# Kernel tuning notes

Hardware: AMD Instinct MI355X
Metric: run time of the kernel (lower is better)

Reference implementation:

```python
import jax, jax.numpy as jnp
import numpy as np
from jax.ops import segment_sum, segment_max

N = 20000      # nodes
DEG = 16       # incoming edges per node
E = N * DEG    # edges
IN = 128       # in_features
BOND = 16      # bond_features_dim
OUT = 128      # output_features
NUM_LAYERS = 3
LEAKY = 0.2
ELU_ALPHA = 1.0


def _lin_params(key, out_f, in_f):
    kw, kb = jax.random.split(key)
    s = 1.0 / np.sqrt(in_f)
    w = jax.random.uniform(kw, (out_f, in_f), jnp.float32, -s, s)
    b = jax.random.uniform(kb, (out_f,), jnp.float32, -s, s)
    return w, b


def setup_inputs() -> dict:
    key = jax.random.key(0)
    ks = jax.random.split(key, 20)
    atom_features = jax.random.normal(ks[0], (N, IN), jnp.float32)
    edge_src = jax.random.randint(ks[1], (E,), 0, N, jnp.int32)
    # every node receives exactly DEG edges (avoids the isolated-node bug path)
    edge_dst = jnp.repeat(jnp.arange(N, dtype=jnp.int32), DEG)
    bond_features = jax.random.normal(ks[2], (E, BOND), jnp.float32)

    v1_fc1_w, v1_fc1_b = _lin_params(ks[3], OUT, IN)
    v1_fc2_w, v1_fc2_b = _lin_params(ks[4], OUT, IN + BOND)
    v1_att_w, v1_att_b = _lin_params(ks[5], 1, 2 * OUT)
    v1_attend_w, v1_attend_b = _lin_params(ks[6], OUT, OUT)
    v1_gru_wih, v1_gru_bih = _lin_params(ks[7], 3 * OUT, OUT)
    v1_gru_whh, v1_gru_bhh = _lin_params(ks[8], 3 * OUT, OUT)

    v2_fc1_w, v2_fc1_b = _lin_params(ks[9], 1, 2 * OUT)
    v2_fc2_w, v2_fc2_b = _lin_params(ks[10], OUT, OUT)
    v2_gru_wih, v2_gru_bih = _lin_params(ks[11], 3 * OUT, OUT)
    v2_gru_whh, v2_gru_bhh = _lin_params(ks[12], 3 * OUT, OUT)

    lin_w, lin_b = _lin_params(ks[13], OUT, OUT)

    return dict(atom_features=atom_features, edge_src=edge_src, edge_dst=edge_dst,
                bond_features=bond_features,
                v1_fc1_w=v1_fc1_w, v1_fc1_b=v1_fc1_b, v1_fc2_w=v1_fc2_w, v1_fc2_b=v1_fc2_b,
                v1_att_w=v1_att_w, v1_att_b=v1_att_b, v1_attend_w=v1_attend_w, v1_attend_b=v1_attend_b,
                v1_gru_wih=v1_gru_wih, v1_gru_whh=v1_gru_whh, v1_gru_bih=v1_gru_bih, v1_gru_bhh=v1_gru_bhh,
                v2_fc1_w=v2_fc1_w, v2_fc1_b=v2_fc1_b, v2_fc2_w=v2_fc2_w, v2_fc2_b=v2_fc2_b,
                v2_gru_wih=v2_gru_wih, v2_gru_whh=v2_gru_whh, v2_gru_bih=v2_gru_bih, v2_gru_bhh=v2_gru_bhh,
                lin_w=lin_w, lin_b=lin_b)


def _linear(x, w, b):
    return x @ w.T + b


def _gru_cell(x, h, wih, whh, bih, bhh):
    gi = x @ wih.T + bih   # [N, 3*OUT]
    gh = h @ whh.T + bhh
    i_r, i_z, i_n = jnp.split(gi, 3, axis=-1)
    h_r, h_z, h_n = jnp.split(gh, 3, axis=-1)
    r = jax.nn.sigmoid(i_r + h_r)
    z = jax.nn.sigmoid(i_z + h_z)
    n = jnp.tanh(i_n + r * h_n)
    return (1.0 - z) * n + z * h


def _segment_softmax(logits, seg, n):
    m = segment_max(logits, seg, num_segments=n)
    ex = jnp.exp(logits - m[seg])
    den = segment_sum(ex, seg, num_segments=n)
    return ex / den[seg]


def reference(atom_features, edge_src, edge_dst, bond_features,
              v1_fc1_w, v1_fc1_b, v1_fc2_w, v1_fc2_b, v1_att_w, v1_att_b,
              v1_attend_w, v1_attend_b, v1_gru_wih, v1_gru_whh, v1_gru_bih, v1_gru_bhh,
              v2_fc1_w, v2_fc1_b, v2_fc2_w, v2_fc2_b,
              v2_gru_wih, v2_gru_whh, v2_gru_bih, v2_gru_bhh,
              lin_w, lin_b):
    n = atom_features.shape[0]
    lrelu = lambda x: jax.nn.leaky_relu(x, negative_slope=LEAKY)

    # ---- GATlayerV1 ----
    new_atom = lrelu(_linear(atom_features, v1_fc1_w, v1_fc1_b))           # [N, OUT]
    nbr_trans = _linear(new_atom, v1_attend_w, v1_attend_b)                # [N, OUT]
    nbr_in = jnp.concatenate([atom_features[edge_src], bond_features], axis=1)  # [E, IN+BOND]
    nbr = lrelu(_linear(nbr_in, v1_fc2_w, v1_fc2_b))                       # [E, OUT]
    pair = jnp.concatenate([new_atom[edge_dst], nbr], axis=1)              # [E, 2*OUT]
    logits = lrelu(_linear(pair, v1_att_w, v1_att_b))[:, 0]                # [E]
    score = _segment_softmax(logits, edge_dst, n)                          # [E]
    transform = segment_sum(score[:, None] * nbr_trans[edge_src], edge_dst, num_segments=n)
    ctx = jax.nn.elu(transform, alpha=ELU_ALPHA)
    h = _gru_cell(ctx, new_atom, v1_gru_wih, v1_gru_whh, v1_gru_bih, v1_gru_bhh)
    G_0 = new_atom

    all_tensors = [h]

    # ---- GATlayerV2 (shared weights across layers 2..NUM_LAYERS) ----
    for _ in range(NUM_LAYERS - 1):
        nt = _linear(h, v2_fc2_w, v2_fc2_b)                                # [N, OUT]
        pair2 = jnp.concatenate([h[edge_dst], h[edge_src]], axis=1)        # [E, 2*OUT]
        lg = lrelu(_linear(pair2, v2_fc1_w, v2_fc1_b))[:, 0]               # [E]
        sc = _segment_softmax(lg, edge_dst, n)
        tr = segment_sum(sc[:, None] * nt[edge_src], edge_dst, num_segments=n)
        ctx2 = jax.nn.elu(tr, alpha=ELU_ALPHA)
        h = _gru_cell(ctx2, h, v2_gru_wih, v2_gru_whh, v2_gru_bih, v2_gru_bhh)
        all_tensors.append(h)

    all_stack = jnp.stack(all_tensors)           # [NUM_LAYERS, N, OUT]
    averaged = all_stack.mean(axis=0)            # [N, OUT]
    output = jax.nn.gelu(_linear(averaged, lin_w, lin_b), approximate=False)
    return (output, all_stack, G_0, averaged)
```

## Files before the change

### kernel.cpp

```cpp
#include <hip/hip_runtime.h>
#include <math.h>

#define NN 20000
#define EE 320000

using short8 = __attribute__((ext_vector_type(8))) short;
using f32x4  = __attribute__((ext_vector_type(4))) float;
using u16x4  = __attribute__((ext_vector_type(4))) unsigned short;

__device__ __forceinline__ unsigned short f2bf(float x) {
    union { float f; unsigned u; } v; v.f = x;
    unsigned r = (v.u + 0x7fffu + ((v.u >> 16) & 1u)) >> 16;
    return (unsigned short)r;
}
__device__ __forceinline__ float bf2f(unsigned short b) {
    union { unsigned u; float f; } v; v.u = ((unsigned)b) << 16;
    return v.f;
}
__device__ __forceinline__ float sigmoidf_(float x) { return 1.f / (1.f + __expf(-x)); }
__device__ __forceinline__ float tanhf_(float x) {
    float e = __expf(-2.f * x);
    return (1.f - e) / (1.f + e);
}
__device__ __forceinline__ float lrelu_(float x) { return x > 0.f ? x : 0.2f * x; }
__device__ __forceinline__ float elu_(float x) { return x > 0.f ? x : __expf(x) - 1.f; }

struct PackDesc { const float* w; unsigned short* out; int O; int ldw; int mode; };
struct PackArgs { PackDesc d[10]; };

__global__ void k_pack(PackArgs args) {
    PackDesc d = args.d[blockIdx.y];
    int idx = blockIdx.x * 256 + threadIdx.x;
    if (d.mode == 1) {
        if (idx >= 512) return;
        int t = idx >> 6, l = idx & 63;
        int lr = l & 15, lg = l >> 4;
        int ch = lr * 8 + t;
        short8 o;
        #pragma unroll
        for (int j = 0; j < 8; j++) {
            int k = lg * 8 + j;
            o[j] = (k < 16) ? (short)f2bf(d.w[(size_t)ch * 144 + 128 + k]) : (short)0;
        }
        *(short8*)(d.out + (size_t)idx * 8) = o;
        return;
    }
    int total = (d.O / 16) * 4 * 64;
    if (idx >= total) return;
    int l = idx & 63, rest = idx >> 6;
    int ko = rest & 3, no = rest >> 2;
    int row = no * 16 + (l & 15);
    int col0 = ko * 32 + ((l >> 4) * 8);
    const float* src = d.w + (size_t)row * d.ldw + col0;
    unsigned short o[8];
    #pragma unroll
    for (int j = 0; j < 8; j++) o[j] = f2bf(src[j]);
    #pragma unroll
    for (int j = 0; j < 8; j++) d.out[(size_t)idx * 8 + j] = o[j];
}

__global__ __launch_bounds__(256) void k_v1_front(
    const float* __restrict__ atom,
    const unsigned short* __restrict__ Bfc1, const unsigned short* __restrict__ BW2a,
    const float* __restrict__ fc1_b, const float* __restrict__ fc2_b,
    const float* __restrict__ attw,
    float* __restrict__ g0, unsigned short* __restrict__ naBf,
    unsigned short* __restrict__ Ubf, float* __restrict__ adst)
{
    __shared__ float Xs[16][132];
    __shared__ unsigned short Ys2[16 * 128];
    const int tid = threadIdx.x, l = tid & 63, w = tid >> 6;
    const int lr = l & 15, lg = l >> 4;
    const int m0 = blockIdx.x * 16;

    f32x4 acc1[2] = {}, accU[2] = {};
    #pragma unroll
    for (int ko = 0; ko < 4; ko++) {
        const f32x4* ap = (const f32x4*)(atom + (size_t)(m0 + lr) * 128 + ko * 32 + lg * 8);
        f32x4 a0 = ap[0], a1 = ap[1];
        short8 af;
        #pragma unroll
        for (int j = 0; j < 4; j++) { af[j] = (short)f2bf(a0[j]); af[4 + j] = (short)f2bf(a1[j]); }
        #pragma unroll
        for (int i = 0; i < 2; i++) {
            int t = w * 2 + i;
            short8 b1 = *(const short8*)(Bfc1 + ((size_t)(t * 4 + ko) * 64 + l) * 8);
            acc1[i] = __builtin_amdgcn_mfma_f32_16x16x32_bf16(af, b1, acc1[i], 0, 0, 0);
            short8 bu = *(const short8*)(BW2a + ((size_t)(t * 4 + ko) * 64 + l) * 8);
            accU[i] = __builtin_amdgcn_mfma_f32_16x16x32_bf16(af, bu, accU[i], 0, 0, 0);
        }
    }
    #pragma unroll
    for (int i = 0; i < 2; i++) {
        int col = (w * 2 + i) * 16 + lr;
        float b1v = fc1_b[col], bUv = fc2_b[col];
        #pragma unroll
        for (int r = 0; r < 4; r++) {
            int row = lg * 4 + r;
            float v = lrelu_(acc1[i][r] + b1v);
            Xs[row][col] = v;
            Ys2[row * 128 + col] = f2bf(accU[i][r] + bUv);
        }
    }
    __syncthreads();
    *(short8*)(Ubf + (size_t)m0 * 128 + tid * 8) = *(const short8*)(Ys2 + tid * 8);
    {
        int row = tid >> 4, q = tid & 15;
        short8 tmp;
        float p = 0.f;
        float vv[8];
        #pragma unroll
        for (int j = 0; j < 8; j++) {
            float x = Xs[row][q * 8 + j];
            vv[j] = x;
            tmp[j] = (short)f2bf(x);
            p = fmaf(x, attw[q * 8 + j], p);
        }
        *(f32x4*)(g0 + (size_t)(m0 + row) * 128 + q * 8) = *(f32x4*)vv;
        *(f32x4*)(g0 + (size_t)(m0 + row) * 128 + q * 8 + 4) = *(f32x4*)(vv + 4);
        *(short8*)(naBf + (size_t)(m0 + row) * 128 + q * 8) = tmp;
        #pragma unroll
        for (int m = 1; m <= 8; m <<= 1) p += __shfl_xor(p, m, 16);
        if (q == 0) adst[m0 + row] = p;
    }
}

template<int AGGMODE, int FRONT, int FINAL>
__global__ __launch_bounds__(512, 4) void k_gru(
    const float* __restrict__ aD, const float* __restrict__ bS, const float* __restrict__ b1,
    const float* __restrict__ bond, const unsigned short* __restrict__ BW2b,
    const float* __restrict__ attw, const float* __restrict__ attb1,
    const float* __restrict__ adst, const unsigned short* __restrict__ U,
    const int* __restrict__ esrc, const unsigned short* __restrict__ V,
    const unsigned short* __restrict__ Bpre, const float* __restrict__ bpre,
    const unsigned short* __restrict__ Bih, const unsigned short* __restrict__ Bhh,
    const float* __restrict__ bih, const float* __restrict__ bhh,
    const unsigned short* __restrict__ hprevBf, float* __restrict__ houtF,
    unsigned short* __restrict__ houtBf,
    const float* __restrict__ w2att, float* __restrict__ aDOut, float* __restrict__ bSOut,
    const float* __restrict__ as0, const float* __restrict__ as1,
    const unsigned short* __restrict__ Blin, const float* __restrict__ linb,
    float* __restrict__ avgOut, float* __restrict__ outF)
{
    __shared__ unsigned short aggS[32][136];
    __shared__ unsigned short ctxS[32][136];
    __shared__ unsigned short hpS[32][136];
    __shared__ float hoS[32][132];
    __shared__ float lgS[32][16];
    const int tid = threadIdx.x, l = tid & 63, w = tid >> 6;
    const int lr = l & 15, lg = l >> 4;
    const int m0 = blockIdx.x * 32;
    const int srow = tid >> 4, sc0 = (tid & 15) * 8;

    *(short8*)&hpS[srow][sc0] = *(const short8*)(hprevBf + (size_t)(m0 + srow) * 128 + sc0);

    if (AGGMODE == 0) {
        float aw[8];
        #pragma unroll
        for (int t = 0; t < 8; t++) aw[t] = attw[128 + lr * 8 + t];
        const float ab = attb1[0];
        #pragma unroll
        for (int nn = 0; nn < 4; nn++) {
            const int n = m0 + w * 4 + nn;
            const int e0 = n * 16;
            short8 af = {};
            if (lg < 2) {
                const f32x4* bp = (const f32x4*)(bond + (size_t)(e0 + lr) * 16 + lg * 8);
                f32x4 b0 = bp[0], b1v = bp[1];
                #pragma unroll
                for (int j = 0; j < 4; j++) {
                    af[j] = (short)f2bf(b0[j]); af[4 + j] = (short)f2bf(b1v[j]);
                }
            }
            f32x4 c[8];
            #pragma unroll
            for (int t = 0; t < 8; t++) {
                short8 bw = *(const short8*)(BW2b + (size_t)(t * 64 + l) * 8);
                f32x4 z = {};
                c[t] = __builtin_amdgcn_mfma_f32_16x16x32_bf16(af, bw, z, 0, 0, 0);
            }
            float s[4];
            #pragma unroll
            for (int r = 0; r < 4; r++) {
                int e = e0 + lg * 4 + r;
                int src = esrc[e];
                short8 u = *(const short8*)(U + (size_t)src * 128 + lr * 8);
                float a0 = 0.f;
                #pragma unroll
                for (int t = 0; t < 8; t++)
                    a0 = fmaf(aw[t], lrelu_(c[t][r] + bf2f((unsigned short)u[t])), a0);
                s[r] = a0;
            }
            #pragma unroll
            for (int mk = 1; mk <= 8; mk <<= 1)
                #pragma unroll
                for (int r = 0; r < 4; r++) s[r] += __shfl_xor(s[r], mk, 16);
            if (lr == 0) {
                float anode = adst[n];
                #pragma unroll
                for (int r = 0; r < 4; r++)
                    lgS[w * 4 + nn][lg * 4 + r] = lrelu_(anode + ab + s[r]);
            }
        }
        __syncthreads();
    }

    {
        const int q = tid & 15;
        const int gnode = m0 + srow;
        const int e = gnode * 16 + q;
        const int src = esrc[e];
        float lgt;
        if (AGGMODE == 0) lgt = lgS[srow][q];
        else              lgt = lrelu_(aD[gnode] + bS[src] + b1[0]);
        float mx = lgt;
        #pragma unroll
        for (int mk = 1; mk <= 8; mk <<= 1) mx = fmaxf(mx, __shfl_xor(mx, mk, 16));
        float ex = __expf(lgt - mx);
        float den = ex;
        #pragma unroll
        for (int mk = 1; mk <= 8; mk <<= 1) den += __shfl_xor(den, mk, 16);
        float wq = ex / den;
        float s[8] = {};
        #pragma unroll
        for (int i = 0; i < 16; i++) {
            float wi = __shfl(wq, i, 16);
            int si = __shfl(src, i, 16);
            const unsigned short* vp = V + (size_t)si * 128 + q * 4;
            u16x4 v0 = *(const u16x4*)vp;
            #pragma unroll
            for (int j = 0; j < 4; j++) s[j] = fmaf(wi, bf2f(v0[j]), s[j]);
            u16x4 v1 = *(const u16x4*)(vp + 64);
            #pragma unroll
            for (int j = 0; j < 4; j++) s[4 + j] = fmaf(wi, bf2f(v1[j]), s[4 + j]);
        }
        u16x4 o0, o1;
        #pragma unroll
        for (int j = 0; j < 4; j++) { o0[j] = f2bf(s[j]); o1[j] = f2bf(s[4 + j]); }
        *(u16x4*)&aggS[srow][q * 4] = o0;
        *(u16x4*)&aggS[srow][64 + q * 4] = o1;
    }
    __syncthreads();

    f32x4 accp[2] = {};
    f32x4 ah[2][3] = {};
    #pragma unroll
    for (int ko = 0; ko < 4; ko++) {
        short8 afA[2], afh[2];
        #pragma unroll
        for (int rt = 0; rt < 2; rt++) {
            afA[rt] = *(const short8*)&aggS[rt * 16 + lr][ko * 32 + lg * 8];
            afh[rt] = *(const short8*)&hpS[rt * 16 + lr][ko * 32 + lg * 8];
        }
        short8 bfp = *(const short8*)(Bpre + ((size_t)(w * 4 + ko) * 64 + l) * 8);
        #pragma unroll
        for (int rt = 0; rt < 2; rt++)
            accp[rt] = __builtin_amdgcn_mfma_f32_16x16x32_bf16(afA[rt], bfp, accp[rt], 0, 0, 0);
        #pragma unroll
        for (int g = 0; g < 3; g++) {
            short8 bh = *(const short8*)(Bhh + ((size_t)((w + 8 * g) * 4 + ko) * 64 + l) * 8);
            #pragma unroll
            for (int rt = 0; rt < 2; rt++)
                ah[rt][g] = __builtin_amdgcn_mfma_f32_16x16x32_bf16(afh[rt], bh, ah[rt][g], 0, 0, 0);
        }
    }
    {
        const int col = w * 16 + lr;
        const float bb = bpre[col];
        #pragma unroll
        for (int rt = 0; rt < 2; rt++)
            #pragma unroll
            for (int r = 0; r < 4; r++)
                ctxS[rt * 16 + lg * 4 + r][col] = f2bf(elu_(accp[rt][r] + bb));
    }
    __syncthreads();

    f32x4 ai[2][3] = {};
    #pragma unroll
    for (int ko = 0; ko < 4; ko++) {
        short8 afc[2];
        #pragma unroll
        for (int rt = 0; rt < 2; rt++)
            afc[rt] = *(const short8*)&ctxS[rt * 16 + lr][ko * 32 + lg * 8];
        #pragma unroll
        for (int g = 0; g < 3; g++) {
            short8 bi = *(const short8*)(Bih + ((size_t)((w + 8 * g) * 4 + ko) * 64 + l) * 8);
            #pragma unroll
            for (int rt = 0; rt < 2; rt++)
                ai[rt][g] = __builtin_amdgcn_mfma_f32_16x16x32_bf16(afc[rt], bi, ai[rt][g], 0, 0, 0);
        }
    }
    {
        const int c = w * 16 + lr;
        const float br = bih[c] + bhh[c];
        const float bz = bih[c + 128] + bhh[c + 128];
        const float bin_ = bih[c + 256];
        const float bhn = bhh[c + 256];
        #pragma unroll
        for (int rt = 0; rt < 2; rt++)
            #pragma unroll
            for (int r = 0; r < 4; r++) {
                const int lrow = rt * 16 + lg * 4 + r;
                float rg = sigmoidf_(ai[rt][0][r] + ah[rt][0][r] + br);
                float zg = sigmoidf_(ai[rt][1][r] + ah[rt][1][r] + bz);
                float ng = tanhf_(ai[rt][2][r] + bin_ + rg * (ah[rt][2][r] + bhn));
                float hp = bf2f(hpS[lrow][c]);
                hoS[lrow][c] = fmaf(zg, hp - ng, ng);
            }
    }
    __syncthreads();

    {
        float v[8];
        #pragma unroll
        for (int k = 0; k < 8; k++) v[k] = hoS[srow][sc0 + k];
        f32x4* dst = (f32x4*)(houtF + (size_t)(m0 + srow) * 128 + sc0);
        dst[0] = *(f32x4*)v;
        dst[1] = *(f32x4*)(v + 4);
        if (FINAL == 0) {
            short8 p;
            #pragma unroll
            for (int k = 0; k < 8; k++) p[k] = (short)f2bf(v[k]);
            *(short8*)(houtBf + (size_t)(m0 + srow) * 128 + sc0) = p;
        }
    }

    if (FRONT) {
        int row = tid >> 4, q = tid & 15;
        float pa = 0.f, pb = 0.f;
        #pragma unroll
        for (int j = 0; j < 8; j++) {
            float x = hoS[row][q * 8 + j];
            pa = fmaf(x, w2att[q * 8 + j], pa);
            pb = fmaf(x, w2att[128 + q * 8 + j], pb);
        }
        #pragma unroll
        for (int m = 1; m <= 8; m <<= 1) {
            pa += __shfl_xor(pa, m, 16);
            pb += __shfl_xor(pb, m, 16);
        }
        if (q == 0) { aDOut[m0 + row] = pa; bSOut[m0 + row] = pb; }
    }

    if (FINAL) {
        {
            const f32x4* p0 = (const f32x4*)(as0 + (size_t)(m0 + srow) * 128 + sc0);
            const f32x4* p1 = (const f32x4*)(as1 + (size_t)(m0 + srow) * 128 + sc0);
            f32x4* pav = (f32x4*)(avgOut + (size_t)(m0 + srow) * 128 + sc0);
            #pragma unroll
            for (int k = 0; k < 2; k++) {
                f32x4 x0 = p0[k], x1 = p1[k];
                f32x4 av;
                #pragma unroll
                for (int j = 0; j < 4; j++)
                    av[j] = (x0[j] + x1[j] + hoS[srow][sc0 + k * 4 + j]) * (1.f / 3.f);
                pav[k] = av;
                #pragma unroll
                for (int j = 0; j < 4; j++) ctxS[srow][sc0 + k * 4 + j] = f2bf(av[j]);
            }
        }
        __syncthreads();
        f32x4 acc2[2] = {};
        #pragma unroll
        for (int ko = 0; ko < 4; ko++) {
            short8 bf = *(const short8*)(Blin + ((size_t)(w * 4 + ko) * 64 + l) * 8);
            #pragma unroll
            for (int rt = 0; rt < 2; rt++) {
                short8 af = *(const short8*)&ctxS[rt * 16 + lr][ko * 32 + lg * 8];
                acc2[rt] = __builtin_amdgcn_mfma_f32_16x16x32_bf16(af, bf, acc2[rt], 0, 0, 0);
            }
        }
        __syncthreads();
        {
            const int col = w * 16 + lr;
            const float bb = linb[col];
            #pragma unroll
            for (int rt = 0; rt < 2; rt++)
                #pragma unroll
                for (int r = 0; r < 4; r++) {
                    float vv = acc2[rt][r] + bb;
                    hoS[rt * 16 + lg * 4 + r][col] =
                        0.5f * vv * (1.f + erff(vv * 0.70710678118654752f));
                }
        }
        __syncthreads();
        {
            float v[8];
            #pragma unroll
            for (int k = 0; k < 8; k++) v[k] = hoS[srow][sc0 + k];
            f32x4* dst = (f32x4*)(outF + (size_t)(m0 + srow) * 128 + sc0);
            dst[0] = *(f32x4*)v;
            dst[1] = *(f32x4*)(v + 4);
        }
    }
}

extern "C" void kernel_launch(void* const* d_in, const int* in_sizes, int n_in,
                              void* d_out, int out_size, void* d_ws, size_t ws_size,
                              hipStream_t stream) {
    const float* atom     = (const float*)d_in[0];
    const int*   esrc     = (const int*)d_in[1];
    const float* bond     = (const float*)d_in[3];
    const float* fc1_w    = (const float*)d_in[4];
    const float* fc1_b    = (const float*)d_in[5];
    const float* fc2_w    = (const float*)d_in[6];
    const float* fc2_b    = (const float*)d_in[7];
    const float* att_w    = (const float*)d_in[8];
    const float* att_b    = (const float*)d_in[9];
    const float* attend_w = (const float*)d_in[10];
    const float* attend_b = (const float*)d_in[11];
    const float* gih1     = (const float*)d_in[12];
    const float* ghh1     = (const float*)d_in[13];
    const float* bih1     = (const float*)d_in[14];
    const float* bhh1     = (const float*)d_in[15];
    const float* fc1v2_w  = (const float*)d_in[16];
    const float* fc1v2_b  = (const float*)d_in[17];
    const float* fc2v2_w  = (const float*)d_in[18];
    const float* fc2v2_b  = (const float*)d_in[19];
    const float* gih2     = (const float*)d_in[20];
    const float* ghh2     = (const float*)d_in[21];
    const float* bih2     = (const float*)d_in[22];
    const float* bhh2     = (const float*)d_in[23];
    const float* lin_w    = (const float*)d_in[24];
    const float* lin_b    = (const float*)d_in[25];

    char* wsb = (char*)d_ws;
    size_t off = 0;
    auto allocB = [&](size_t bytes) {
        size_t o = off; off = (off + bytes + 255) & ~(size_t)255; return o;
    };
    unsigned short* Bfc1   = (unsigned short*)(wsb + allocB(128 * 128 * 2));
    unsigned short* Batt   = (unsigned short*)(wsb + allocB(128 * 128 * 2));
    unsigned short* BW2a   = (unsigned short*)(wsb + allocB(128 * 128 * 2));
    unsigned short* BW2b   = (unsigned short*)(wsb + allocB(512 * 8 * 2));
    unsigned short* Bgih1  = (unsigned short*)(wsb + allocB(384 * 128 * 2));
    unsigned short* Bghh1  = (unsigned short*)(wsb + allocB(384 * 128 * 2));
    unsigned short* Bfc2v2 = (unsigned short*)(wsb + allocB(128 * 128 * 2));
    unsigned short* Bgih2  = (unsigned short*)(wsb + allocB(384 * 128 * 2));
    unsigned short* Bghh2  = (unsigned short*)(wsb + allocB(384 * 128 * 2));
    unsigned short* Blin   = (unsigned short*)(wsb + allocB(128 * 128 * 2));
    unsigned short* naBf   = (unsigned short*)(wsb + allocB((size_t)NN * 128 * 2));
    unsigned short* Ubf    = (unsigned short*)(wsb + allocB((size_t)NN * 128 * 2));
    unsigned short* h1Bf   = (unsigned short*)(wsb + allocB((size_t)NN * 128 * 2));
    unsigned short* h2Bf   = (unsigned short*)(wsb + allocB((size_t)NN * 128 * 2));
    float* adst   = (float*)(wsb + allocB((size_t)NN * 4));
    float* aD     = (float*)(wsb + allocB((size_t)NN * 4));
    float* bS     = (float*)(wsb + allocB((size_t)NN * 4));
    (void)ws_size;

    float* out0 = (float*)d_out;
    float* as0  = out0 + (size_t)NN * 128;
    float* as1  = as0 + (size_t)NN * 128;
    float* as2  = as1 + (size_t)NN * 128;
    float* g0   = out0 + (size_t)4 * NN * 128;
    float* avg  = out0 + (size_t)5 * NN * 128;

    PackArgs pa;
    pa.d[0] = { fc1_w,    Bfc1,   128, 128, 0 };
    pa.d[1] = { attend_w, Batt,   128, 128, 0 };
    pa.d[2] = { fc2_w,    BW2a,   128, 144, 0 };
    pa.d[3] = { gih1,     Bgih1,  384, 128, 0 };
    pa.d[4] = { ghh1,     Bghh1,  384, 128, 0 };
    pa.d[5] = { fc2v2_w,  Bfc2v2, 128, 128, 0 };
    pa.d[6] = { gih2,     Bgih2,  384, 128, 0 };
    pa.d[7] = { ghh2,     Bghh2,  384, 128, 0 };
    pa.d[8] = { lin_w,    Blin,   128, 128, 0 };
    pa.d[9] = { fc2_w,    BW2b,   0,   0,   1 };
    k_pack<<<dim3(24, 10), 256, 0, stream>>>(pa);

    const int GB = NN / 16;
    const int GB32 = NN / 32;

    k_v1_front<<<GB, 256, 0, stream>>>(atom, Bfc1, BW2a, fc1_b, fc2_b, att_w,
                                       g0, naBf, Ubf, adst);
    k_gru<0, 1, 0><<<GB32, 512, 0, stream>>>(
        nullptr, nullptr, nullptr,
        bond, BW2b, att_w, att_b, adst, Ubf,
        esrc, naBf,
        Batt, attend_b,
        Bgih1, Bghh1, bih1, bhh1, naBf, as0, h1Bf,
        fc1v2_w, aD, bS,
        nullptr, nullptr, nullptr, nullptr, nullptr, nullptr);

    k_gru<1, 1, 0><<<GB32, 512, 0, stream>>>(
        aD, bS, fc1v2_b,
        nullptr, nullptr, nullptr, nullptr, nullptr, nullptr,
        esrc, h1Bf,
        Bfc2v2, fc2v2_b,
        Bgih2, Bghh2, bih2, bhh2, h1Bf, as1, h2Bf,
        fc1v2_w, aD, bS,
        nullptr, nullptr, nullptr, nullptr, nullptr, nullptr);

    k_gru<1, 0, 1><<<GB32, 512, 0, stream>>>(
        aD, bS, fc1v2_b,
        nullptr, nullptr, nullptr, nullptr, nullptr, nullptr,
        esrc, h2Bf,
        Bfc2v2, fc2v2_b,
        Bgih2, Bghh2, bih2, bhh2, h2Bf, as2, nullptr,
        nullptr, nullptr, nullptr,
        as0, as1, Blin, lin_b, avg, out0);
}
```

Before: 123.3 us.

## Halve GRU kernel node tile to 16 rows and drop fp32 staging buffer

Each k_gru block now processes 16 nodes instead of 32 with 512 threads, so twice as many blocks launch, registers per thread drop, and launch bounds request 8 blocks per CU. The fp32 hoS shared buffer is removed: the GRU output is written back into hpS as bf16 and reused for outputs, attention projections and the final linear. The aim is higher occupancy and less LDS per block to hide gather latency. The cost is that hidden states and the final output are rounded to bf16 before being written as fp32, which lowers precision, and weight-fragment loads are amortised over fewer rows.

```diff
diff --git a/kernel.cpp b/kernel.cpp
--- a/kernel.cpp
+++ b/kernel.cpp
@@ -126,7 +126,7 @@
 }
 
 template<int AGGMODE, int FRONT, int FINAL>
-__global__ __launch_bounds__(512, 4) void k_gru(
+__global__ __launch_bounds__(512, 8) void k_gru(
     const float* __restrict__ aD, const float* __restrict__ bS, const float* __restrict__ b1,
     const float* __restrict__ bond, const unsigned short* __restrict__ BW2b,
     const float* __restrict__ attw, const float* __restrict__ attb1,
@@ -142,17 +142,16 @@
     const unsigned short* __restrict__ Blin, const float* __restrict__ linb,
     float* __restrict__ avgOut, float* __restrict__ outF)
 {
-    __shared__ unsigned short aggS[32][136];
-    __shared__ unsigned short ctxS[32][136];
-    __shared__ unsigned short hpS[32][136];
-    __shared__ float hoS[32][132];
-    __shared__ float lgS[32][16];
+    __shared__ unsigned short aggS[16][136];
+    __shared__ unsigned short ctxS[16][136];
+    __shared__ unsigned short hpS[16][136];
+    __shared__ float lgS[(AGGMODE == 0) ? 16 : 1][16];
     const int tid = threadIdx.x, l = tid & 63, w = tid >> 6;
     const int lr = l & 15, lg = l >> 4;
-    const int m0 = blockIdx.x * 32;
-    const int srow = tid >> 4, sc0 = (tid & 15) * 8;
-
-    *(short8*)&hpS[srow][sc0] = *(const short8*)(hprevBf + (size_t)(m0 + srow) * 128 + sc0);
+    const int m0 = blockIdx.x * 16;
+    const int r2 = tid >> 5, c4 = (tid & 31) * 4;
+
+    *(u16x4*)&hpS[r2][c4] = *(const u16x4*)(hprevBf + (size_t)(m0 + r2) * 128 + c4);
 
     if (AGGMODE == 0) {
         float aw[8];
@@ -160,8 +159,8 @@
         for (int t = 0; t < 8; t++) aw[t] = attw[128 + lr * 8 + t];
         const float ab = attb1[0];
         #pragma unroll
-        for (int nn = 0; nn < 4; nn++) {
-            const int n = m0 + w * 4 + nn;
+        for (int nn = 0; nn < 2; nn++) {
+            const int n = m0 + w * 2 + nn;
             const int e0 = n * 16;
             short8 af = {};
             if (lg < 2) {
@@ -199,19 +198,22 @@
                 float anode = adst[n];
                 #pragma unroll
                 for (int r = 0; r < 4; r++)
-                    lgS[w * 4 + nn][lg * 4 + r] = lrelu_(anode + ab + s[r]);
+                    lgS[w * 2 + nn][lg * 4 + r] = lrelu_(anode + ab + s[r]);
             }
         }
         __syncthreads();
     }
 
     {
-        const int q = tid & 15;
-        const int gnode = m0 + srow;
+        const int g2 = tid >> 5;
+        const int q2 = tid & 31;
+        const int q = q2 & 15;
+        const int hf = q2 >> 4;
+        const int gnode = m0 + g2;
         const int e = gnode * 16 + q;
         const int src = esrc[e];
         float lgt;
-        if (AGGMODE == 0) lgt = lgS[srow][q];
+        if (AGGMODE == 0) lgt = lgS[g2][q];
         else              lgt = lrelu_(aD[gnode] + bS[src] + b1[0]);
         float mx = lgt;
         #pragma unroll
@@ -221,73 +223,53 @@
         #pragma unroll
         for (int mk = 1; mk <= 8; mk <<= 1) den += __shfl_xor(den, mk, 16);
         float wq = ex / den;
-        float s[8] = {};
+        float s[4] = {};
         #pragma unroll
         for (int i = 0; i < 16; i++) {
             float wi = __shfl(wq, i, 16);
             int si = __shfl(src, i, 16);
-            const unsigned short* vp = V + (size_t)si * 128 + q * 4;
-            u16x4 v0 = *(const u16x4*)vp;
-            #pragma unroll
-            for (int j = 0; j < 4; j++) s[j] = fmaf(wi, bf2f(v0[j]), s[j]);
-            u16x4 v1 = *(const u16x4*)(vp + 64);
-            #pragma unroll
-            for (int j = 0; j < 4; j++) s[4 + j] = fmaf(wi, bf2f(v1[j]), s[4 + j]);
-        }
-        u16x4 o0, o1;
-        #pragma unroll
-        for (int j = 0; j < 4; j++) { o0[j] = f2bf(s[j]); o1[j] = f2bf(s[4 + j]); }
-        *(u16x4*)&aggS[srow][q * 4] = o0;
-        *(u16x4*)&aggS[srow][64 + q * 4] = o1;
+            u16x4 v = *(const u16x4*)(V + (size_t)si * 128 + hf * 64 + q * 4);
+            #pragma unroll
+            for (int j = 0; j < 4; j++) s[j] = fmaf(wi, bf2f(v[j]), s[j]);
+        }
+        u16x4 o;
+        #pragma unroll
+        for (int j = 0; j < 4; j++) o[j] = f2bf(s[j]);
+        *(u16x4*)&aggS[g2][hf * 64 + q * 4] = o;
     }
     __syncthreads();
 
-    f32x4 accp[2] = {};
-    f32x4 ah[2][3] = {};
+    f32x4 accp = {};
+    f32x4 ah[3] = {};
     #pragma unroll
     for (int ko = 0; ko < 4; ko++) {
-        short8 afA[2], afh[2];
-        #pragma unroll
-        for (int rt = 0; rt < 2; rt++) {
-            afA[rt] = *(const short8*)&aggS[rt * 16 + lr][ko * 32 + lg * 8];
-            afh[rt] = *(const short8*)&hpS[rt * 16 + lr][ko * 32 + lg * 8];
-        }
+        short8 afA = *(const short8*)&aggS[lr][ko * 32 + lg * 8];
+        short8 afh = *(const short8*)&hpS[lr][ko * 32 + lg * 8];
         short8 bfp = *(const short8*)(Bpre + ((size_t)(w * 4 + ko) * 64 + l) * 8);
-        #pragma unroll
-        for (int rt = 0; rt < 2; rt++)
-            accp[rt] = __builtin_amdgcn_mfma_f32_16x16x32_bf16(afA[rt], bfp, accp[rt], 0, 0, 0);
+        accp = __builtin_amdgcn_mfma_f32_16x16x32_bf16(afA, bfp, accp, 0, 0, 0);
         #pragma unroll
         for (int g = 0; g < 3; g++) {
             short8 bh = *(const short8*)(Bhh + ((size_t)((w + 8 * g) * 4 + ko) * 64 + l) * 8);
-            #pragma unroll
-            for (int rt = 0; rt < 2; rt++)
-                ah[rt][g] = __builtin_amdgcn_mfma_f32_16x16x32_bf16(afh[rt], bh, ah[rt][g], 0, 0, 0);
+            ah[g] = __builtin_amdgcn_mfma_f32_16x16x32_bf16(afh, bh, ah[g], 0, 0, 0);
         }
     }
     {
         const int col = w * 16 + lr;
         const float bb = bpre[col];
         #pragma unroll
-        for (int rt = 0; rt < 2; rt++)
-            #pragma unroll
-            for (int r = 0; r < 4; r++)
-                ctxS[rt * 16 + lg * 4 + r][col] = f2bf(elu_(accp[rt][r] + bb));
+        for (int r = 0; r < 4; r++)
+            ctxS[lg * 4 + r][col] = f2bf(elu_(accp[r] + bb));
     }
     __syncthreads();
 
-    f32x4 ai[2][3] = {};
+    f32x4 ai[3] = {};
     #pragma unroll
     for (int ko = 0; ko < 4; ko++) {
-        short8 afc[2];
-        #pragma unroll
-        for (int rt = 0; rt < 2; rt++)
-            afc[rt] = *(const short8*)&ctxS[rt * 16 + lr][ko * 32 + lg * 8];
+        short8 afc = *(const short8*)&ctxS[lr][ko * 32 + lg * 8];
         #pragma unroll
         for (int g = 0; g < 3; g++) {
             short8 bi = *(const short8*)(Bih + ((size_t)((w + 8 * g) * 4 + ko) * 64 + l) * 8);
-            #pragma unroll
-            for (int rt = 0; rt < 2; rt++)
-                ai[rt][g] = __builtin_amdgcn_mfma_f32_16x16x32_bf16(afc[rt], bi, ai[rt][g], 0, 0, 0);
+            ai[g] = __builtin_amdgcn_mfma_f32_16x16x32_bf16(afc, bi, ai[g], 0, 0, 0);
         }
     }
     {
@@ -297,100 +279,87 @@
         const float bin_ = bih[c + 256];
         const float bhn = bhh[c + 256];
         #pragma unroll
-        for (int rt = 0; rt < 2; rt++)
-            #pragma unroll
-            for (int r = 0; r < 4; r++) {
-                const int lrow = rt * 16 + lg * 4 + r;
-                float rg = sigmoidf_(ai[rt][0][r] + ah[rt][0][r] + br);
-                float zg = sigmoidf_(ai[rt][1][r] + ah[rt][1][r] + bz);
-                float ng = tanhf_(ai[rt][2][r] + bin_ + rg * (ah[rt][2][r] + bhn));
-                float hp = bf2f(hpS[lrow][c]);
-                hoS[lrow][c] = fmaf(zg, hp - ng, ng);
-            }
+        for (int r = 0; r < 4; r++) {
+            const int lrow = lg * 4 + r;
+            float rg = sigmoidf_(ai[0][r] + ah[0][r] + br);
+            float zg = sigmoidf_(ai[1][r] + ah[1][r] + bz);
+            float ng = tanhf_(ai[2][r] + bin_ + rg * (ah[2][r] + bhn));
+            float hp = bf2f(hpS[lrow][c]);
+            hpS[lrow][c] = f2bf(fmaf(zg, hp - ng, ng));
+        }
     }
     __syncthreads();
 
     {
-        float v[8];
-        #pragma unroll
-        for (int k = 0; k < 8; k++) v[k] = hoS[srow][sc0 + k];
-        f32x4* dst = (f32x4*)(houtF + (size_t)(m0 + srow) * 128 + sc0);
-        dst[0] = *(f32x4*)v;
-        dst[1] = *(f32x4*)(v + 4);
-        if (FINAL == 0) {
-            short8 p;
-            #pragma unroll
-            for (int k = 0; k < 8; k++) p[k] = (short)f2bf(v[k]);
-            *(short8*)(houtBf + (size_t)(m0 + srow) * 128 + sc0) = p;
-        }
+        u16x4 hv = *(const u16x4*)&hpS[r2][c4];
+        f32x4 vf;
+        #pragma unroll
+        for (int j = 0; j < 4; j++) vf[j] = bf2f(hv[j]);
+        *(f32x4*)(houtF + (size_t)(m0 + r2) * 128 + c4) = vf;
+        if (FINAL == 0)
+            *(u16x4*)(houtBf + (size_t)(m0 + r2) * 128 + c4) = hv;
     }
 
     if (FRONT) {
-        int row = tid >> 4, q = tid & 15;
-        float pa = 0.f, pb = 0.f;
-        #pragma unroll
-        for (int j = 0; j < 8; j++) {
-            float x = hoS[row][q * 8 + j];
-            pa = fmaf(x, w2att[q * 8 + j], pa);
-            pb = fmaf(x, w2att[128 + q * 8 + j], pb);
-        }
-        #pragma unroll
-        for (int m = 1; m <= 8; m <<= 1) {
-            pa += __shfl_xor(pa, m, 16);
-            pb += __shfl_xor(pb, m, 16);
-        }
-        if (q == 0) { aDOut[m0 + row] = pa; bSOut[m0 + row] = pb; }
+        if (tid < 256) {
+            int row = tid >> 4, q = tid & 15;
+            short8 hv8 = *(const short8*)&hpS[row][q * 8];
+            float pa = 0.f, pb = 0.f;
+            #pragma unroll
+            for (int j = 0; j < 8; j++) {
+                float x = bf2f((unsigned short)hv8[j]);
+                pa = fmaf(x, w2att[q * 8 + j], pa);
+                pb = fmaf(x, w2att[128 + q * 8 + j], pb);
+            }
+            #pragma unroll
+            for (int m = 1; m <= 8; m <<= 1) {
+                pa += __shfl_xor(pa, m, 16);
+                pb += __shfl_xor(pb, m, 16);
+            }
+            if (q == 0) { aDOut[m0 + row] = pa; bSOut[m0 + row] = pb; }
+        }
     }
 
     if (FINAL) {
         {
-            const f32x4* p0 = (const f32x4*)(as0 + (size_t)(m0 + srow) * 128 + sc0);
-            const f32x4* p1 = (const f32x4*)(as1 + (size_t)(m0 + srow) * 128 + sc0);
-            f32x4* pav = (f32x4*)(avgOut + (size_t)(m0 + srow) * 128 + sc0);
-            #pragma unroll
-            for (int k = 0; k < 2; k++) {
-                f32x4 x0 = p0[k], x1 = p1[k];
-                f32x4 av;
-                #pragma unroll
-                for (int j = 0; j < 4; j++)
-                    av[j] = (x0[j] + x1[j] + hoS[srow][sc0 + k * 4 + j]) * (1.f / 3.f);
-                pav[k] = av;
-                #pragma unroll
-                for (int j = 0; j < 4; j++) ctxS[srow][sc0 + k * 4 + j] = f2bf(av[j]);
-            }
+            f32x4 x0 = *(const f32x4*)(as0 + (size_t)(m0 + r2) * 128 + c4);
+            f32x4 x1 = *(const f32x4*)(as1 + (size_t)(m0 + r2) * 128 + c4);
+            u16x4 hv = *(const u16x4*)&hpS[r2][c4];
+            f32x4 av;
+            #pragma unroll
+            for (int j = 0; j < 4; j++)
+                av[j] = (x0[j] + x1[j] + bf2f(hv[j])) * (1.f / 3.f);
+            *(f32x4*)(avgOut + (size_t)(m0 + r2) * 128 + c4) = av;
+            u16x4 ab16;
+            #pragma unroll
+            for (int j = 0; j < 4; j++) ab16[j] = f2bf(av[j]);
+            *(u16x4*)&ctxS[r2][c4] = ab16;
         }
         __syncthreads();
-        f32x4 acc2[2] = {};
+        f32x4 acc2 = {};
         #pragma unroll
         for (int ko = 0; ko < 4; ko++) {
+            short8 af = *(const short8*)&ctxS[lr][ko * 32 + lg * 8];
             short8 bf = *(const short8*)(Blin + ((size_t)(w * 4 + ko) * 64 + l) * 8);
-            #pragma unroll
-            for (int rt = 0; rt < 2; rt++) {
-                short8 af = *(const short8*)&ctxS[rt * 16 + lr][ko * 32 + lg * 8];
-                acc2[rt] = __builtin_amdgcn_mfma_f32_16x16x32_bf16(af, bf, acc2[rt], 0, 0, 0);
-            }
-        }
-        __syncthreads();
+            acc2 = __builtin_amdgcn_mfma_f32_16x16x32_bf16(af, bf, acc2, 0, 0, 0);
+        }
         {
             const int col = w * 16 + lr;
             const float bb = linb[col];
             #pragma unroll
-            for (int rt = 0; rt < 2; rt++)
-                #pragma unroll
-                for (int r = 0; r < 4; r++) {
-                    float vv = acc2[rt][r] + bb;
-                    hoS[rt * 16 + lg * 4 + r][col] =
-                        0.5f * vv * (1.f + erff(vv * 0.70710678118654752f));
-                }
+            for (int r = 0; r < 4; r++) {
+                float vv = acc2[r] + bb;
+                vv = 0.5f * vv * (1.f + erff(vv * 0.70710678118654752f));
+                aggS[lg * 4 + r][col] = f2bf(vv);
+            }
         }
         __syncthreads();
         {
-            float v[8];
-            #pragma unroll
-            for (int k = 0; k < 8; k++) v[k] = hoS[srow][sc0 + k];
-            f32x4* dst = (f32x4*)(outF + (size_t)(m0 + srow) * 128 + sc0);
-            dst[0] = *(f32x4*)v;
-            dst[1] = *(f32x4*)(v + 4);
+            u16x4 ov = *(const u16x4*)&aggS[r2][c4];
+            f32x4 vf;
+            #pragma unroll
+            for (int j = 0; j < 4; j++) vf[j] = bf2f(ov[j]);
+            *(f32x4*)(outF + (size_t)(m0 + r2) * 128 + c4) = vf;
         }
     }
 }
@@ -469,11 +438,10 @@
     k_pack<<<dim3(24, 10), 256, 0, stream>>>(pa);
 
     const int GB = NN / 16;
-    const int GB32 = NN / 32;
 
     k_v1_front<<<GB, 256, 0, stream>>>(atom, Bfc1, BW2a, fc1_b, fc2_b, att_w,
                                        g0, naBf, Ubf, adst);
-    k_gru<0, 1, 0><<<GB32, 512, 0, stream>>>(
+    k_gru<0, 1, 0><<<GB, 512, 0, stream>>>(
         nullptr, nullptr, nullptr,
         bond, BW2b, att_w, att_b, adst, Ubf,
         esrc, naBf,
@@ -482,7 +450,7 @@
         fc1v2_w, aD, bS,
         nullptr, nullptr, nullptr, nullptr, nullptr, nullptr);
 
-    k_gru<1, 1, 0><<<GB32, 512, 0, stream>>>(
+    k_gru<1, 1, 0><<<GB, 512, 0, stream>>>(
         aD, bS, fc1v2_b,
         nullptr, nullptr, nullptr, nullptr, nullptr, nullptr,
         esrc, h1Bf,
@@ -491,7 +459,7 @@
         fc1v2_w, aD, bS,
         nullptr, nullptr, nullptr, nullptr, nullptr, nullptr);
 
-    k_gru<1, 0, 1><<<GB32, 512, 0, stream>>>(
+    k_gru<1, 0, 1><<<GB, 512, 0, stream>>>(
         aD, bS, fc1v2_b,
         nullptr, nullptr, nullptr, nullptr, nullptr, nullptr,
         esrc, h2Bf,
```

Result: slower. 138.4 us (+12.3%).
